# Kernel optimization log

Hardware: AMD Instinct MI355X
Metric: run time of the kernel (lower is better)

The kernel has to match this reference:

```python
import jax, jax.numpy as jnp
import numpy as np

STEP_SIZE = 0.3333          # module default self.step_size
N_STEPS = 4                 # >= ceil(halfWidth/step) for sigma=6, size_factor=1; extra steps are masked to 0
REF_SIZE = 1024.0           # IndexHelper.input_size_factor() reference resolution


def _bilinear(img, px, py):
    """Bilinear sample img [B,C,H,W] at normalized coords px,py [B,H,W] in [0,1].
    Pixel centers at (j+0.5)/W (grid_sample align_corners=False convention); border clamp."""
    B, C, H, W = img.shape
    fx = px * W - 0.5
    fy = py * H - 0.5
    x0 = jnp.floor(fx)
    y0 = jnp.floor(fy)
    wx = (fx - x0)[:, None]  # [B,1,H,W]
    wy = (fy - y0)[:, None]
    x0i = jnp.clip(x0.astype(jnp.int32), 0, W - 1)
    x1i = jnp.clip(x0i + 1, 0, W - 1)
    y0i = jnp.clip(y0.astype(jnp.int32), 0, H - 1)
    y1i = jnp.clip(y0i + 1, 0, H - 1)
    gather = jax.vmap(lambda im, yi, xi: im[:, yi, xi])  # per-batch advanced indexing -> [B,C,H,W]
    v00 = gather(img, y0i, x0i)
    v01 = gather(img, y0i, x1i)
    v10 = gather(img, y1i, x0i)
    v11 = gather(img, y1i, x1i)
    top = v00 * (1.0 - wx) + v01 * wx
    bot = v10 * (1.0 - wx) + v11 * wx
    return top * (1.0 - wy) + bot * wy


def _forward(x, tangent, sigma):
    B, C, H, W = x.shape
    dt = x.dtype
    size_factor = min(H, W) / REF_SIZE           # i.input_size_factor()
    sig = sigma.reshape(-1, 1, 1, 1) * size_factor  # precisionFactor = 1.0
    half_width = 2.0 * sig
    two_sigma2 = 2.0 * sig * sig
    step = 1.0 / (STEP_SIZE * size_factor)       # step = i.view(1/step_size), mode=None scaling

    # p_start: normalized pixel-center coords, channel 0 = x (width), channel 1 = y (height)
    ys, xs = jnp.meshgrid((jnp.arange(H, dtype=dt) + 0.5) / H,
                          (jnp.arange(W, dtype=dt) + 0.5) / W, indexing="ij")
    p_start = jnp.broadcast_to(jnp.stack([xs, ys])[None], (B, 2, H, W))
    tex = jnp.array([W, H], dtype=dt).reshape(1, 2, 1, 1)  # i.tex_size()

    def march(direction):
        v0 = direction
        p0 = p_start + v0 / tex

        def body(carry, it):
            c, c_sum, p, v = carry
            r = (it + 1.0) * step                       # r = step, step+step, ...
            k = jnp.exp(-r * r / two_sigma2)            # [B,1,1,1]
            k = jnp.where(r < half_width, k, 0.0)
            px, py = p[:, 0], p[:, 1]
            inb = (px >= 0.0) & (px < 1.0) & (py >= 0.0) & (py < 1.0)
            k = k * inb[:, None].astype(dt)             # [B,1,H,W]
            c = c + _bilinear(x, px, py) * k
            c_sum = c_sum + k
            tf = _bilinear(tangent, px, py)
            vt = jnp.sum(v * tf, axis=1, keepdims=True)
            tf = jnp.where(vt < 0.0, -tf, tf)           # keep marching direction consistent
            p = p + tf / tex
            return (c, c_sum, p, tf), None

        init = (jnp.zeros_like(x), jnp.zeros((B, 1, H, W), dt), p0, v0)
        (c, c_sum, _, _), _ = jax.lax.scan(body, init, jnp.arange(N_STEPS, dtype=dt))
        return c, c_sum

    c1, s1 = march(tangent)      # smoothed(C, Sum, tangent_sampled)
    c2, s2 = march(-tangent)     # smoothed(C, Sum, -tangent_sampled)
    return (x + c1 + c2) / (1.0 + s1 + s2)


def setup_inputs() -> dict:
    key = jax.random.key(0)
    k1, k2 = jax.random.split(key)
    B, C, H, W = 2, 3, 1024, 1024
    x = jax.random.normal(k1, (B, C, H, W), jnp.float32)
    # tangent: unit-length per-pixel flow direction field
    theta = jax.random.uniform(k2, (B, 1, H, W), jnp.float32, 0.0, 2.0 * np.pi)
    tangent = jnp.concatenate([jnp.cos(theta), jnp.sin(theta)], axis=1)
    sigma = jnp.full((B,), 6.0, jnp.float32)  # smoothing width in pixels
    return {"x": x, "tangent": tangent, "sigma": sigma}


def reference(x, tangent, sigma):
    return _forward(x, tangent, sigma)
```

## Files before the change

### kernel.cpp

```cpp
#include <hip/hip_runtime.h>

constexpr int Bb = 2, Cc = 3, Hh = 1024, Ww = 1024;
constexpr int HWp = Hh * Ww;
constexpr int N_STEPS = 4;
constexpr int TS = 16;
constexpr int HALO = 6;
constexpr int TD = TS + 2 * HALO;
constexpr int TSTR = TD + 1;

struct Corn { int o00, o01, o10, o11; float wx, wy; };

__device__ __forceinline__ Corn mkcorn(float px, float py, int ox, int oy) {
#pragma clang fp contract(off)
    float fx = px * 1024.0f - 0.5f;
    float fy = py * 1024.0f - 0.5f;
    float fx0 = floorf(fx), fy0 = floorf(fy);
    Corn c;
    c.wx = fx - fx0;
    c.wy = fy - fy0;
    int x0 = (int)fx0, y0 = (int)fy0;
    int x0i = min(max(x0, 0), Ww - 1);
    int x1i = min(x0i + 1, Ww - 1);
    int y0i = min(max(y0, 0), Hh - 1);
    int y1i = min(y0i + 1, Hh - 1);
    int lx0 = min(max(x0i - ox, 0), TD - 1);
    int lx1 = min(max(x1i - ox, 0), TD - 1);
    int ly0 = min(max(y0i - oy, 0), TD - 1);
    int ly1 = min(max(y1i - oy, 0), TD - 1);
    c.o00 = ly0 * TSTR + lx0; c.o01 = ly0 * TSTR + lx1;
    c.o10 = ly1 * TSTR + lx0; c.o11 = ly1 * TSTR + lx1;
    return c;
}

__device__ __forceinline__ float bsamp(const float* p, const Corn& c) {
#pragma clang fp contract(off)
    float v00 = p[c.o00], v01 = p[c.o01], v10 = p[c.o10], v11 = p[c.o11];
    float omx = 1.0f - c.wx, omy = 1.0f - c.wy;
    float top = v00 * omx + v01 * c.wx;
    float bot = v10 * omx + v11 * c.wx;
    return top * omy + bot * c.wy;
}

__global__ __launch_bounds__(256) void flow_smooth_kernel(
    const float* __restrict__ x,
    const float* __restrict__ tg,
    const float* __restrict__ sg,
    float* __restrict__ out)
{
#pragma clang fp contract(off)
    __shared__ float lds[5][TD * TSTR];

    const int tx0 = blockIdx.x * TS, ty0 = blockIdx.y * TS;
    const int b = blockIdx.z;
    const int tid = threadIdx.x;

    const float* xp  = x  + (size_t)b * Cc * HWp;
    const float* txp = tg + (size_t)b * 2 * HWp;
    const float* typ = txp + HWp;
    const float* planes[5] = { xp, xp + HWp, xp + 2 * HWp, txp, typ };

    const int ox = tx0 - HALO, oy = ty0 - HALO;

    for (int e = tid; e < TD * TD; e += 256) {
        int r = e / TD, cc = e - r * TD;
        int gy = min(max(oy + r, 0), Hh - 1);
        int gx = min(max(ox + cc, 0), Ww - 1);
        int g = gy * Ww + gx;
#pragma unroll
        for (int pl = 0; pl < 5; ++pl)
            lds[pl][r * TSTR + cc] = planes[pl][g];
    }
    __syncthreads();

    const int lx = tid & (TS - 1), ly = tid >> 4;
    const int j = tx0 + lx, i = ty0 + ly;
    const int ctr = (HALO + ly) * TSTR + (HALO + lx);

    float sig = sg[b];
    float half_width = 2.0f * sig;
    float two_sigma2 = (2.0f * sig) * sig;
    const float stepf = (float)(1.0 / 0.3333);

    float ks[N_STEPS];
#pragma unroll
    for (int it = 0; it < N_STEPS; ++it) {
        float r = ((float)it + 1.0f) * stepf;
        float k = expf(-(r * r) / two_sigma2);
        ks[it] = (r < half_width) ? k : 0.0f;
    }

    const float inv1024 = 1.0f / 1024.0f;
    const float psx = ((float)j + 0.5f) * inv1024;
    const float psy = ((float)i + 0.5f) * inv1024;

    float v0x = lds[3][ctr];
    float v0y = lds[4][ctr];

    float c1a = 0.f, c1b = 0.f, c1c = 0.f, s1 = 0.f;
    float c2a = 0.f, c2b = 0.f, c2c = 0.f, s2 = 0.f;

#pragma unroll
    for (int d = 0; d < 2; ++d) {
        float vx = d ? -v0x : v0x;
        float vy = d ? -v0y : v0y;
        float px = psx + vx * inv1024;
        float py = psy + vy * inv1024;
        float a0 = 0.f, a1 = 0.f, a2 = 0.f, as = 0.f;
#pragma unroll
        for (int it = 0; it < N_STEPS; ++it) {
            Corn c = mkcorn(px, py, ox, oy);
            bool inb = (px >= 0.0f) && (px < 1.0f) && (py >= 0.0f) && (py < 1.0f);
            float w = inb ? ks[it] : 0.0f;
            a0 += bsamp(lds[0], c) * w;
            a1 += bsamp(lds[1], c) * w;
            a2 += bsamp(lds[2], c) * w;
            as += w;
            if (it == N_STEPS - 1) break;
            float tfx = bsamp(lds[3], c);
            float tfy = bsamp(lds[4], c);
            float vt = (vx * tfx) + (vy * tfy);
            if (vt < 0.0f) { tfx = -tfx; tfy = -tfy; }
            px = px + tfx * inv1024;
            py = py + tfy * inv1024;
            vx = tfx; vy = tfy;
        }
        if (d == 0) { c1a = a0; c1b = a1; c1c = a2; s1 = as; }
        else        { c2a = a0; c2b = a1; c2c = a2; s2 = as; }
    }

    const int pix = i * Ww + j;
    float xc0 = lds[0][ctr], xc1 = lds[1][ctr], xc2 = lds[2][ctr];
    float denom = (1.0f + s1) + s2;
    float* op = out + (size_t)b * Cc * HWp;
    op[pix]           = ((xc0 + c1a) + c2a) / denom;
    op[pix + HWp]     = ((xc1 + c1b) + c2b) / denom;
    op[pix + 2 * HWp] = ((xc2 + c1c) + c2c) / denom;
}

extern "C" void kernel_launch(void* const* d_in, const int* in_sizes, int n_in,
                              void* d_out, int out_size, void* d_ws, size_t ws_size,
                              hipStream_t stream) {
    const float* x = nullptr; const float* tg = nullptr; const float* sg = nullptr;
    for (int t = 0; t < n_in; ++t) {
        if (in_sizes[t] == Bb * Cc * HWp)      x  = (const float*)d_in[t];
        else if (in_sizes[t] == Bb * 2 * HWp)  tg = (const float*)d_in[t];
        else                                   sg = (const float*)d_in[t];
    }
    float* out = (float*)d_out;

    dim3 block(256, 1, 1);
    dim3 grid(Ww / TS, Hh / TS, Bb);
    flow_smooth_kernel<<<grid, block, 0, stream>>>(x, tg, sg, out);
}
```

Measured before the change: 139.7 us.

## Specialize interior tiles to skip clamping and switch to pixel-space coordinates

Splits the kernel into border and interior template variants. Interior tiles skip the global and local index clamping and bounds checks, and compute the four corner offsets from a single base offset. Coordinates are now kept in pixel units instead of being normalized by 1024. Steps whose kernel weight is zero skip the colour sampling. Risks: the unclamped interior path assumes the march never leaves the halo, and removing the 1024 scaling may change rounding slightly.

```diff
diff --git a/kernel.cpp b/kernel.cpp
--- a/kernel.cpp
+++ b/kernel.cpp
@@ -8,63 +8,85 @@
 constexpr int TD = TS + 2 * HALO;
 constexpr int TSTR = TD + 1;
 
-struct Corn { int o00, o01, o10, o11; float wx, wy; };
+struct Corn { int o00, o01, o10, o11; float wx, wy, omx, omy; };
 
-__device__ __forceinline__ Corn mkcorn(float px, float py, int ox, int oy) {
+__device__ __forceinline__ Corn mkcorn_int(float px, float py, int ox, int oy) {
 #pragma clang fp contract(off)
-    float fx = px * 1024.0f - 0.5f;
-    float fy = py * 1024.0f - 0.5f;
+    float fx = px - 0.5f;
+    float fy = py - 0.5f;
     float fx0 = floorf(fx), fy0 = floorf(fy);
     Corn c;
-    c.wx = fx - fx0;
-    c.wy = fy - fy0;
+    c.wx = fx - fx0;  c.wy = fy - fy0;
+    c.omx = 1.0f - c.wx;  c.omy = 1.0f - c.wy;
+    int o = ((int)fy0 - oy) * TSTR + ((int)fx0 - ox);
+    c.o00 = o;        c.o01 = o + 1;
+    c.o10 = o + TSTR; c.o11 = o + TSTR + 1;
+    return c;
+}
+
+__device__ __forceinline__ Corn mkcorn_bor(float px, float py, int ox, int oy) {
+#pragma clang fp contract(off)
+    float fx = px - 0.5f;
+    float fy = py - 0.5f;
+    float fx0 = floorf(fx), fy0 = floorf(fy);
+    Corn c;
+    c.wx = fx - fx0;  c.wy = fy - fy0;
+    c.omx = 1.0f - c.wx;  c.omy = 1.0f - c.wy;
     int x0 = (int)fx0, y0 = (int)fy0;
     int x0i = min(max(x0, 0), Ww - 1);
     int x1i = min(x0i + 1, Ww - 1);
     int y0i = min(max(y0, 0), Hh - 1);
     int y1i = min(y0i + 1, Hh - 1);
-    int lx0 = min(max(x0i - ox, 0), TD - 1);
-    int lx1 = min(max(x1i - ox, 0), TD - 1);
-    int ly0 = min(max(y0i - oy, 0), TD - 1);
-    int ly1 = min(max(y1i - oy, 0), TD - 1);
-    c.o00 = ly0 * TSTR + lx0; c.o01 = ly0 * TSTR + lx1;
-    c.o10 = ly1 * TSTR + lx0; c.o11 = ly1 * TSTR + lx1;
+    int lx0 = x0i - ox, lx1 = x1i - ox;
+    int ly0 = y0i - oy, ly1 = y1i - oy;
+    c.o00 = ly0 * TSTR + lx0;  c.o01 = ly0 * TSTR + lx1;
+    c.o10 = ly1 * TSTR + lx0;  c.o11 = ly1 * TSTR + lx1;
     return c;
 }
 
 __device__ __forceinline__ float bsamp(const float* p, const Corn& c) {
 #pragma clang fp contract(off)
     float v00 = p[c.o00], v01 = p[c.o01], v10 = p[c.o10], v11 = p[c.o11];
-    float omx = 1.0f - c.wx, omy = 1.0f - c.wy;
-    float top = v00 * omx + v01 * c.wx;
-    float bot = v10 * omx + v11 * c.wx;
-    return top * omy + bot * c.wy;
+    float top = v00 * c.omx + v01 * c.wx;
+    float bot = v10 * c.omx + v11 * c.wx;
+    return top * c.omy + bot * c.wy;
 }
 
-__global__ __launch_bounds__(256) void flow_smooth_kernel(
-    const float* __restrict__ x,
-    const float* __restrict__ tg,
-    const float* __restrict__ sg,
-    float* __restrict__ out)
+template <bool BORDER>
+__device__ __forceinline__ void run_tile(
+    const float* __restrict__ x, const float* __restrict__ tg,
+    const float* __restrict__ sg, float* __restrict__ out,
+    float (&lds)[5][TD * TSTR])
 {
 #pragma clang fp contract(off)
-    __shared__ float lds[5][TD * TSTR];
-
     const int tx0 = blockIdx.x * TS, ty0 = blockIdx.y * TS;
     const int b = blockIdx.z;
     const int tid = threadIdx.x;
 
     const float* xp  = x  + (size_t)b * Cc * HWp;
     const float* txp = tg + (size_t)b * 2 * HWp;
-    const float* typ = txp + HWp;
-    const float* planes[5] = { xp, xp + HWp, xp + 2 * HWp, txp, typ };
+    const float* planes[5] = { xp, xp + HWp, xp + 2 * HWp, txp, txp + HWp };
+    const int ox = tx0 - HALO, oy = ty0 - HALO;
 
-    const int ox = tx0 - HALO, oy = ty0 - HALO;
+    float sig = sg[b];
+    float half_width = 2.0f * sig;
+    float two_sigma2 = (2.0f * sig) * sig;
+    const float stepf = (float)(1.0 / 0.3333);
+    float ks[N_STEPS];
+#pragma unroll
+    for (int it = 0; it < N_STEPS; ++it) {
+        float r = ((float)it + 1.0f) * stepf;
+        float k = expf(-(r * r) / two_sigma2);
+        ks[it] = (r < half_width) ? k : 0.0f;
+    }
 
     for (int e = tid; e < TD * TD; e += 256) {
         int r = e / TD, cc = e - r * TD;
-        int gy = min(max(oy + r, 0), Hh - 1);
-        int gx = min(max(ox + cc, 0), Ww - 1);
+        int gy = oy + r, gx = ox + cc;
+        if (BORDER) {
+            gy = min(max(gy, 0), Hh - 1);
+            gx = min(max(gx, 0), Ww - 1);
+        }
         int g = gy * Ww + gx;
 #pragma unroll
         for (int pl = 0; pl < 5; ++pl)
@@ -76,22 +98,8 @@
     const int j = tx0 + lx, i = ty0 + ly;
     const int ctr = (HALO + ly) * TSTR + (HALO + lx);
 
-    float sig = sg[b];
-    float half_width = 2.0f * sig;
-    float two_sigma2 = (2.0f * sig) * sig;
-    const float stepf = (float)(1.0 / 0.3333);
-
-    float ks[N_STEPS];
-#pragma unroll
-    for (int it = 0; it < N_STEPS; ++it) {
-        float r = ((float)it + 1.0f) * stepf;
-        float k = expf(-(r * r) / two_sigma2);
-        ks[it] = (r < half_width) ? k : 0.0f;
-    }
-
-    const float inv1024 = 1.0f / 1024.0f;
-    const float psx = ((float)j + 0.5f) * inv1024;
-    const float psy = ((float)i + 0.5f) * inv1024;
+    const float psx = (float)j + 0.5f;
+    const float psy = (float)i + 0.5f;
 
     float v0x = lds[3][ctr];
     float v0y = lds[4][ctr];
@@ -103,25 +111,32 @@
     for (int d = 0; d < 2; ++d) {
         float vx = d ? -v0x : v0x;
         float vy = d ? -v0y : v0y;
-        float px = psx + vx * inv1024;
-        float py = psy + vy * inv1024;
+        float px = psx + vx;
+        float py = psy + vy;
         float a0 = 0.f, a1 = 0.f, a2 = 0.f, as = 0.f;
 #pragma unroll
         for (int it = 0; it < N_STEPS; ++it) {
-            Corn c = mkcorn(px, py, ox, oy);
-            bool inb = (px >= 0.0f) && (px < 1.0f) && (py >= 0.0f) && (py < 1.0f);
-            float w = inb ? ks[it] : 0.0f;
-            a0 += bsamp(lds[0], c) * w;
-            a1 += bsamp(lds[1], c) * w;
-            a2 += bsamp(lds[2], c) * w;
-            as += w;
+            Corn c = BORDER ? mkcorn_bor(px, py, ox, oy)
+                            : mkcorn_int(px, py, ox, oy);
+            if (ks[it] != 0.0f) {
+                float w = ks[it];
+                if (BORDER) {
+                    bool inb = (px >= 0.0f) && (px < 1024.0f) &&
+                               (py >= 0.0f) && (py < 1024.0f);
+                    w = inb ? w : 0.0f;
+                }
+                a0 += bsamp(lds[0], c) * w;
+                a1 += bsamp(lds[1], c) * w;
+                a2 += bsamp(lds[2], c) * w;
+                as += w;
+            }
             if (it == N_STEPS - 1) break;
             float tfx = bsamp(lds[3], c);
             float tfy = bsamp(lds[4], c);
             float vt = (vx * tfx) + (vy * tfy);
             if (vt < 0.0f) { tfx = -tfx; tfy = -tfy; }
-            px = px + tfx * inv1024;
-            py = py + tfy * inv1024;
+            px = px + tfx;
+            py = py + tfy;
             vx = tfx; vy = tfy;
         }
         if (d == 0) { c1a = a0; c1b = a1; c1c = a2; s1 = as; }
@@ -135,6 +150,19 @@
     op[pix]           = ((xc0 + c1a) + c2a) / denom;
     op[pix + HWp]     = ((xc1 + c1b) + c2b) / denom;
     op[pix + 2 * HWp] = ((xc2 + c1c) + c2c) / denom;
+}
+
+__global__ __launch_bounds__(256) void flow_smooth_kernel(
+    const float* __restrict__ x,
+    const float* __restrict__ tg,
+    const float* __restrict__ sg,
+    float* __restrict__ out)
+{
+    __shared__ float lds[5][TD * TSTR];
+    const bool border = (blockIdx.x == 0) || (blockIdx.x == gridDim.x - 1) ||
+                        (blockIdx.y == 0) || (blockIdx.y == gridDim.y - 1);
+    if (border) run_tile<true >(x, tg, sg, out, lds);
+    else        run_tile<false>(x, tg, sg, out, lds);
 }
 
 extern "C" void kernel_launch(void* const* d_in, const int* in_sizes, int n_in,
```

After: 123.2 us. 11.8% less time.
